# Optimization experiments

Measured on AMD Instinct MI355X. Metric: run time of the kernel, lower is better.

The kernel has to match this reference:

```python
import jax, jax.numpy as jnp
import numpy as np

D_MODEL = 1024
N_BLOCK = 20
EPS = 1e-8


def setup_inputs() -> dict:
    key = jax.random.key(0)
    k = jax.random.split(key, 7)
    B, S, D, NB = 8, 2048, D_MODEL, N_BLOCK
    e = jax.random.normal(k[0], (B, S, D), dtype=jnp.float32)
    m = jax.random.normal(k[1], (B, S, D), dtype=jnp.float32)
    state = jax.random.normal(k[2], (1, NB * D), dtype=jnp.float32)
    # learned params of the EntNet-style RNN_cell
    U = jax.random.normal(k[3], (D, D), dtype=jnp.float32) * 0.02
    V = jax.random.normal(k[4], (D, D), dtype=jnp.float32) * 0.02
    W = jax.random.normal(k[5], (D, D), dtype=jnp.float32) * 0.02
    keys = jax.random.normal(k[6], (NB, D), dtype=jnp.float32) * 0.02
    return {"e": e, "m": m, "state": state, "U": U, "V": V, "W": W, "keys": keys}


def reference(e, m, state, U, V, W, keys):
    B, S, D = e.shape
    NB = keys.shape[0]
    h0 = state.reshape(NB, D)  # shared initial memory state across batch
    x = e + m  # combined per-timestep input, (B, S, D)

    def step(h, xt):  # h: (NB, D), xt: (D,)
        # per-slot gate: content similarity + key similarity
        g = jax.nn.sigmoid(h @ xt + keys @ xt)  # (NB,)
        # candidate memory
        cand = jnp.tanh(h @ U.T + keys @ V.T + (W @ xt)[None, :])  # (NB, D)
        h = h + g[:, None] * cand
        # per-slot L2 normalization
        h = h / (jnp.linalg.norm(h, axis=1, keepdims=True) + EPS)
        return h, None

    def run(xseq):  # xseq: (S, D) -> final state (NB, D)
        hT, _ = jax.lax.scan(step, h0, xseq)
        return hT

    out = jax.vmap(run)(x)  # (B, NB, D)
    return out
```

## Files before the change

kernel.cpp:

```cpp
#include <hip/hip_runtime.h>
#include <cstdint>
#include <cstddef>

namespace {

constexpr int D   = 1024;
constexpr int NB  = 20;
constexpr int B   = 8;
constexpr int S   = 2048;
constexpr int NWG = 32;
constexpr float EPS = 1e-8f;

typedef __attribute__((ext_vector_type(4))) float f4_t;
typedef __attribute__((ext_vector_type(8))) short s8_t;
typedef unsigned long long u64_t;

__device__ __forceinline__ unsigned short f2bf(float f) {
  unsigned u = __float_as_uint(f);
  u += 0x7fffu + ((u >> 16) & 1u);
  return (unsigned short)(u >> 16);
}
__device__ __forceinline__ float bf2f(unsigned short h) {
  return __uint_as_float(((unsigned)h) << 16);
}
__device__ __forceinline__ float u64lo(u64_t x) { return __uint_as_float((unsigned)x); }
__device__ __forceinline__ float u64hi(u64_t x) { return __uint_as_float((unsigned)(x >> 32)); }
__device__ __forceinline__ float rcp_f(float x) { return __builtin_amdgcn_rcpf(x); }
__device__ __forceinline__ float sigm_fast(float x) { return rcp_f(1.0f + __expf(-x)); }
__device__ __forceinline__ float tanh_fast(float x) {
  const float e = __expf(2.0f * x);
  return 1.0f - 2.0f * rcp_f(e + 1.0f);
}

#define MFMA(a, b, c) __builtin_amdgcn_mfma_f32_16x16x32_bf16((a), (b), (c), 0, 0, 0)
#define ALOAD64(p) __hip_atomic_load((p), __ATOMIC_RELAXED, __HIP_MEMORY_SCOPE_AGENT)
#define ASTORE64(p, v) __hip_atomic_store((p), (v), __ATOMIC_RELAXED, __HIP_MEMORY_SCOPE_AGENT)
#define ALOAD32(p) __hip_atomic_load((p), __ATOMIC_RELAXED, __HIP_MEMORY_SCOPE_AGENT)
#define ASTORE32(p, v) __hip_atomic_store((p), (v), __ATOMIC_RELAXED, __HIP_MEMORY_SCOPE_AGENT)

constexpr size_t OFF_HBUF = 0;
constexpr size_t OFF_NORM = OFF_HBUF + 2ull * B * NB * 512 * 4;
constexpr size_t OFF_CTR  = OFF_NORM + 2ull * B * NB * NWG * 4;
constexpr size_t OFF_KV   = OFF_CTR + (size_t)B * 32 * 4;
constexpr size_t OFF_KX   = OFF_KV + (size_t)NB * D * 4;
constexpr size_t OFF_UHI  = OFF_KX + (size_t)B * S * NB * 4;
constexpr size_t OFF_ULO  = OFF_UHI + (size_t)D * D * 2;
constexpr size_t OFF_WHI  = OFF_ULO + (size_t)D * D * 2;
constexpr size_t OFF_WLO  = OFF_WHI + (size_t)D * D * 2;


__global__ void k_convert(const float* __restrict__ U, const float* __restrict__ W,
                          unsigned short* __restrict__ Uhi, unsigned short* __restrict__ Ulo,
                          unsigned short* __restrict__ Whi, unsigned short* __restrict__ Wlo) {
  const int n = D * D;
  for (int i = blockIdx.x * blockDim.x + threadIdx.x; i < n; i += gridDim.x * blockDim.x) {
    float u = U[i];
    unsigned short h = f2bf(u);
    Uhi[i] = h;
    Ulo[i] = f2bf(u - bf2f(h));
    float w = W[i];
    h = f2bf(w);
    Whi[i] = h;
    Wlo[i] = f2bf(w - bf2f(h));
  }
}

__global__ void k_kv(const float* __restrict__ keys, const float* __restrict__ V,
                     float* __restrict__ KV) {
  const int tid = threadIdx.x;
  const int j = blockIdx.x * 64 + (tid >> 2);
  const int kq = tid & 3;
  const f4_t* v4 = (const f4_t*)(V + (size_t)j * D + kq * 256);
  const f4_t* k4base = (const f4_t*)keys;
  float acc[NB];
#pragma unroll
  for (int i = 0; i < NB; ++i) acc[i] = 0.f;
  for (int q = 0; q < 64; ++q) {
    const f4_t v = v4[q];
#pragma unroll
    for (int i = 0; i < NB; ++i) {
      const f4_t kk = k4base[i * 256 + kq * 64 + q];
      acc[i] += kk[0] * v[0] + kk[1] * v[1] + kk[2] * v[2] + kk[3] * v[3];
    }
  }
#pragma unroll
  for (int i = 0; i < NB; ++i) {
    float s = acc[i];
    s += __shfl_xor(s, 1);
    s += __shfl_xor(s, 2);
    if (kq == 0) KV[(size_t)i * D + j] = s;
  }
}

__global__ void k_kx(const float* __restrict__ e, const float* __restrict__ m,
                     const float* __restrict__ keys, float* __restrict__ KX) {
  __shared__ f4_t xs[256];
  __shared__ float part[NB][8];
  const int bt = blockIdx.x, tid = threadIdx.x;
  xs[tid] = ((const f4_t*)e)[(size_t)bt * 256 + tid] + ((const f4_t*)m)[(size_t)bt * 256 + tid];
  __syncthreads();
  if (tid < 160) {
    const int i = tid >> 3, s8 = tid & 7;
    float acc = 0.f;
    const f4_t* k4 = (const f4_t*)keys + i * 256 + s8 * 32;
    for (int q = 0; q < 32; ++q) {
      const f4_t kk = k4[q];
      const f4_t xx = xs[s8 * 32 + q];
      acc += kk[0] * xx[0] + kk[1] * xx[1] + kk[2] * xx[2] + kk[3] * xx[3];
    }
    part[i][s8] = acc;
  }
  __syncthreads();
  if (tid < NB) {
    float s = 0.f;
#pragma unroll
    for (int q = 0; q < 8; ++q) s += part[tid][q];
    KX[(size_t)bt * NB + tid] = s;
  }
}

__global__ void k_state(const float* __restrict__ state, unsigned* __restrict__ Hbuf,
                        float* __restrict__ NormP, int* __restrict__ ctr) {
  const int idx = blockIdx.x * 256 + threadIdx.x;
  if (idx < B * NB * 512) {
    const int r = idx % (NB * 512);
    const int i = r >> 9, d2 = (r & 511) << 1;
    const unsigned short a = f2bf(state[i * D + d2]);
    const unsigned short c = f2bf(state[i * D + d2 + 1]);
    Hbuf[idx] = (unsigned)a | ((unsigned)c << 16);
  }
  const int j = idx - B * NB * 512;
  if (j >= 0 && j < B * NB * NWG) NormP[j] = 1.0f / 32.0f;
  const int q = idx - B * NB * 512 - B * NB * NWG;
  if (q >= 0 && q < B * 32) ctr[q] = 0;
}


struct __align__(16) LdsT {
  unsigned short hnA[NB * 1024];
  unsigned short xtA[2][1024];
  float credU[4][2][2][16][20];
  float wxAcc[4][2][16];
  float gAcc[4][2][16];
  float KVs[NB][32];
  float ownH[NB][32];
  float pad_force_1_block_per_cu[3072];
};

__device__ __forceinline__ void build_xt(unsigned short* xt , int tid, f4_t x) {
  const unsigned short h0 = f2bf(x[0]), h1 = f2bf(x[1]), h2 = f2bf(x[2]), h3 = f2bf(x[3]);
  const unsigned short u0 = f2bf(x[0] - bf2f(h0)), u1 = f2bf(x[1] - bf2f(h1));
  const unsigned short u2 = f2bf(x[2] - bf2f(h2)), u3 = f2bf(x[3] - bf2f(h3));
  const int kp = tid << 2;
  *(unsigned*)&xt[kp] = (unsigned)h0 | ((unsigned)h1 << 16);
  *(unsigned*)&xt[kp + 2] = (unsigned)h2 | ((unsigned)h3 << 16);
  *(unsigned*)&xt[1024 + kp] = (unsigned)u0 | ((unsigned)u1 << 16);
  *(unsigned*)&xt[1024 + kp + 2] = (unsigned)u2 | ((unsigned)u3 << 16);
}

__device__ __forceinline__ void stage_h(unsigned short* hn, int tid, const u64_t* hv) {
  const int blkk = tid >> 1;
  const int half = (tid & 1) << 2;
#pragma unroll
  for (int j = 0; j < 20; ++j)
    *(u64_t*)&hn[(j << 10) + ((blkk ^ (j & 15)) << 3) + half] = hv[j];
}

__device__ __forceinline__ void bar_lds() {
  asm volatile("s_waitcnt lgkmcnt(0)\n\ts_barrier" ::: "memory");
}
__device__ __forceinline__ void bar_full() {
  asm volatile("s_waitcnt vmcnt(0) lgkmcnt(0)\n\ts_barrier" ::: "memory");
}

__device__ __forceinline__ void poll8(const unsigned* fb, int wv, int ln, int wg,
                                      unsigned tgt) {
  const int src = (wv << 3) + (ln & 7);
  for (;;) {
    const unsigned v = (src == wg) ? tgt : ALOAD32(fb + src);
    if (__ballot(v >= tgt) == ~0ull) return;
    __builtin_amdgcn_s_sleep(1);
  }
}

__device__ __forceinline__ void poll32(const unsigned* fb, int ln31, int wg,
                                       unsigned tgt, unsigned pv) {
  if (__ballot(pv >= tgt) == ~0ull) return;
  for (;;) {
    const unsigned v = (ln31 == wg) ? tgt : ALOAD32(fb + ln31);
    if (__ballot(v >= tgt) == ~0ull) return;
    __builtin_amdgcn_s_sleep(1);
  }
}

__launch_bounds__(256, 1)
__global__ void k_rnn(const float* __restrict__ e, const float* __restrict__ m,
                      const float* __restrict__ state,
                      const float* __restrict__ KX, const float* __restrict__ KV,
                      const unsigned short* __restrict__ Uhi, const unsigned short* __restrict__ Ulo,
                      const unsigned short* __restrict__ Whi, const unsigned short* __restrict__ Wlo,
                      unsigned* __restrict__ Hbuf, float* __restrict__ NormP,
                      int* __restrict__ ctr, float* __restrict__ out) {
  __shared__ LdsT L;
  const int tid = threadIdx.x;
  const int b = blockIdx.x >> 5;
  const int wg = blockIdx.x & 31;
  const int wv = tid >> 6;
  const int ln = tid & 63;
  const int l15 = ln & 15;
  const int lo4 = ln >> 4;
  const int ln31 = tid & 31;
  const int r1 = 16 + (l15 < 4 ? l15 : 3);
  unsigned* ctrp = (unsigned*)ctr + b * 32;

  const bool uact = (ln < 40);
  const int ui = wv * 5 + (ln >> 3);
  const int uc4 = (ln & 7) << 2;

  s8_t BUh[2][8], BUl[2][8], BWh[2][8], BWl[2][8];
  {
    const int rowb = (wg << 5) + l15;
#pragma unroll
    for (int nt = 0; nt < 2; ++nt)
#pragma unroll
      for (int kf = 0; kf < 8; ++kf) {
        const size_t off = (size_t)(rowb + nt * 16) * D + (wv << 8) + (kf << 5) + (lo4 << 3);
        BUh[nt][kf] = *(const s8_t*)(Uhi + off);
        BUl[nt][kf] = *(const s8_t*)(Ulo + off);
        BWh[nt][kf] = *(const s8_t*)(Whi + off);
        BWl[nt][kf] = *(const s8_t*)(Wlo + off);
      }
  }
  if (tid < 160) {
    const int i = tid >> 3, c4 = (tid & 7) << 2;
    *(f4_t*)&L.ownH[i][c4] = *(const f4_t*)(state + (size_t)i * D + (wg << 5) + c4);
    *(f4_t*)&L.KVs[i][c4] = *(const f4_t*)(KV + (size_t)i * D + (wg << 5) + c4);
  }

  f4_t evv, mvv;
  float sreg = 1.f;
  float kxreg = 0.f;

  s8_t AX[8], A0r[8], A1r[8];
  f4_t cWa0 = {0, 0, 0, 0}, cWa1 = {0, 0, 0, 0};
  f4_t cGa0 = {0, 0, 0, 0}, cGa1 = {0, 0, 0, 0};

  {
    u64_t hv[20];
    const u64_t* hb8 = (const u64_t*)Hbuf + (size_t)(0 * B + b) * (NB * 256);
#pragma unroll
    for (int j = 0; j < 20; ++j) hv[j] = ALOAD64(hb8 + j * 256 + tid);
    const f4_t x0 = ((const f4_t*)e)[(size_t)(b * S) * 256 + tid] +
                    ((const f4_t*)m)[(size_t)(b * S) * 256 + tid];
    build_xt(&L.xtA[0][0], tid, x0);
    stage_h(L.hnA, tid, hv);
    if (uact) kxreg = KX[(size_t)(b * S) * NB + ui];
    evv = ((const f4_t*)e)[(size_t)(b * S + 1) * 256 + tid];
    mvv = ((const f4_t*)m)[(size_t)(b * S + 1) * 256 + tid];
    asm volatile("s_waitcnt lgkmcnt(0)" ::: "memory");
    const unsigned short* xb = &L.xtA[0][0];
    const unsigned short* hb = L.hnA;
#pragma unroll
    for (int kf = 0; kf < 8; ++kf) {
      const int blk = (wv << 5) + (kf << 2) + lo4;
      AX[kf] = *(const s8_t*)&xb[(l15 & 1) * 1024 + (blk << 3)];
      A0r[kf] = *(const s8_t*)&hb[(l15 << 10) + ((blk ^ l15) << 3)];
      A1r[kf] = *(const s8_t*)&hb[(r1 << 10) + ((blk ^ (r1 & 15)) << 3)];
    }
#pragma unroll
    for (int kf = 0; kf < 8; ++kf) {
      cWa0 = MFMA(AX[kf], BWh[0][kf], cWa0);
      cWa0 = MFMA(AX[kf], BWl[0][kf], cWa0);
      cWa1 = MFMA(AX[kf], BWh[1][kf], cWa1);
      cWa1 = MFMA(AX[kf], BWl[1][kf], cWa1);
      cGa0 = MFMA(AX[kf], A0r[kf], cGa0);
      cGa1 = MFMA(AX[kf], A1r[kf], cGa1);
    }
  }
  __syncthreads();

  for (int t = 0; t < S; ++t) {
    const int nxt2 = (t + 1) & 1;

    f4_t cU00 = {0, 0, 0, 0}, cU01 = {0, 0, 0, 0}, cU10 = {0, 0, 0, 0}, cU11 = {0, 0, 0, 0};
#pragma unroll
    for (int kf = 0; kf < 8; ++kf) {
      cU00 = MFMA(A0r[kf], BUh[0][kf], cU00);
      cU00 = MFMA(A0r[kf], BUl[0][kf], cU00);
      cU01 = MFMA(A0r[kf], BUh[1][kf], cU01);
      cU01 = MFMA(A0r[kf], BUl[1][kf], cU01);
      cU10 = MFMA(A1r[kf], BUh[0][kf], cU10);
      cU10 = MFMA(A1r[kf], BUl[0][kf], cU10);
      cU11 = MFMA(A1r[kf], BUh[1][kf], cU11);
      cU11 = MFMA(A1r[kf], BUl[1][kf], cU11);
    }
#pragma unroll
    for (int q = 0; q < 4; ++q) {
      const int r = (lo4 << 2) + q;
      L.credU[wv][0][0][r][l15] = cU00[q];
      L.credU[wv][0][1][r][l15] = cU01[q];
      L.credU[wv][1][0][r][l15] = cU10[q];
      L.credU[wv][1][1][r][l15] = cU11[q];
    }
    if (lo4 == 0) {
      L.wxAcc[wv][0][l15] = cWa0[0] + cWa0[1];
      L.wxAcc[wv][1][l15] = cWa1[0] + cWa1[1];
      L.gAcc[wv][0][l15] = cGa0[0] + cGa0[1];
      L.gAcc[wv][1][l15] = cGa1[0] + cGa1[1];
    }
    bar_lds();

    unsigned pv = 0;
    if (t + 1 < S) pv = (ln31 == wg) ? (unsigned)(t + 1) : ALOAD32(ctrp + ln31);

    if (uact) {
      const int i = ui, c4 = uc4;
      const int mt = i >> 4, r = i & 15, nt = c4 >> 4, ccc = c4 & 15;
      const f4_t sU = *(const f4_t*)&L.credU[0][mt][nt][r][ccc] +
                      *(const f4_t*)&L.credU[1][mt][nt][r][ccc] +
                      *(const f4_t*)&L.credU[2][mt][nt][r][ccc] +
                      *(const f4_t*)&L.credU[3][mt][nt][r][ccc];
      const f4_t wx = *(const f4_t*)&L.wxAcc[0][nt][ccc] +
                      *(const f4_t*)&L.wxAcc[1][nt][ccc] +
                      *(const f4_t*)&L.wxAcc[2][nt][ccc] +
                      *(const f4_t*)&L.wxAcc[3][nt][ccc];
      const f4_t kv = *(const f4_t*)&L.KVs[i][c4];
      const f4_t oh = *(const f4_t*)&L.ownH[i][c4];
      const float s = sreg;
      const float gpre = s * (L.gAcc[0][mt][r] + L.gAcc[1][mt][r] +
                              L.gAcc[2][mt][r] + L.gAcc[3][mt][r]) + kxreg;
      const float g = sigm_fast(gpre);
      f4_t hn;
      float sq = 0.f;
#pragma unroll
      for (int u = 0; u < 4; ++u) {
        const float cand = tanh_fast(s * sU[u] + kv[u] + wx[u]);
        const float hx = s * oh[u] + g * cand;
        hn[u] = hx;
        sq += hx * hx;
      }
      *(f4_t*)&L.ownH[i][c4] = hn;
      const unsigned d0 = (unsigned)f2bf(hn[0]) | ((unsigned)f2bf(hn[1]) << 16);
      const unsigned d1 = (unsigned)f2bf(hn[2]) | ((unsigned)f2bf(hn[3]) << 16);
      u64_t* hb8 = (u64_t*)Hbuf + (size_t)(nxt2 * B + b) * (NB * 256) +
                   (i << 8) + (wg << 3) + (c4 >> 2);
      ASTORE64(hb8, (u64_t)d0 | ((u64_t)d1 << 32));
      sq += __shfl_xor(sq, 1);
      sq += __shfl_xor(sq, 2);
      sq += __shfl_xor(sq, 4);
      if ((ln & 7) == 0) {
        unsigned* np = (unsigned*)NormP + ((size_t)(nxt2 * B + b) * NB + i) * NWG + wg;
        ASTORE32(np, __float_as_uint(sq));
      }
    }
    bar_full();

    if (tid == 0) ASTORE32(ctrp + wg, (unsigned)(t + 1));

    if (t + 1 < S) {
      poll8(ctrp, wv, ln, wg, (unsigned)(t + 1));
      u64_t hv[20];
      const u64_t* g0 = (const u64_t*)Hbuf + (size_t)(nxt2 * B + b) * (NB * 256);
#pragma unroll
      for (int j = 0; j < 20; ++j) hv[j] = ALOAD64(g0 + j * 256 + tid);
      build_xt(&L.xtA[0][0], tid, evv + mvv);
      asm volatile("s_waitcnt lgkmcnt(0)" ::: "memory");
      {
        const unsigned short* xb = &L.xtA[0][0];
#pragma unroll
        for (int kf = 0; kf < 8; ++kf) {
          const int blk = (wv << 5) + (kf << 2) + lo4;
          AX[kf] = *(const s8_t*)&xb[(l15 & 1) * 1024 + (blk << 3)];
        }
        cWa0 = (f4_t){0, 0, 0, 0};
        cWa1 = (f4_t){0, 0, 0, 0};
#pragma unroll
        for (int kf = 0; kf < 8; ++kf) {
          cWa0 = MFMA(AX[kf], BWh[0][kf], cWa0);
          cWa0 = MFMA(AX[kf], BWl[0][kf], cWa0);
          cWa1 = MFMA(AX[kf], BWh[1][kf], cWa1);
          cWa1 = MFMA(AX[kf], BWl[1][kf], cWa1);
        }
      }
      poll32(ctrp, ln31, wg, (unsigned)(t + 1), pv);
      float np0 = 0.f;
      if (uact) {
        const u64_t* n0 = (const u64_t*)NormP + ((size_t)(nxt2 * B + b) * NB + ui) * 16 + ((ln & 7) << 1);
        const u64_t a0 = ALOAD64(n0);
        const u64_t a1 = ALOAD64(n0 + 1);
        np0 = u64lo(a0) + u64hi(a0) + u64lo(a1) + u64hi(a1);
        kxreg = KX[((size_t)b * S + t + 1) * NB + ui];
      }
      stage_h(L.hnA, tid, hv);
      if (t + 2 < S) {
        evv = ((const f4_t*)e)[(size_t)(b * S + t + 2) * 256 + tid];
        mvv = ((const f4_t*)m)[(size_t)(b * S + t + 2) * 256 + tid];
      }
      asm volatile("s_waitcnt lgkmcnt(0)" ::: "memory");
      {
        const unsigned short* hb = L.hnA;
#pragma unroll
        for (int kf = 0; kf < 8; ++kf) {
          const int blk = (wv << 5) + (kf << 2) + lo4;
          A0r[kf] = *(const s8_t*)&hb[(l15 << 10) + ((blk ^ l15) << 3)];
          A1r[kf] = *(const s8_t*)&hb[(r1 << 10) + ((blk ^ (r1 & 15)) << 3)];
        }
        cGa0 = (f4_t){0, 0, 0, 0};
        cGa1 = (f4_t){0, 0, 0, 0};
#pragma unroll
        for (int kf = 0; kf < 8; ++kf) {
          cGa0 = MFMA(AX[kf], A0r[kf], cGa0);
          cGa1 = MFMA(AX[kf], A1r[kf], cGa1);
        }
      }
      if (uact) {
        float s0 = np0;
        s0 += __shfl_xor(s0, 1);
        s0 += __shfl_xor(s0, 2);
        s0 += __shfl_xor(s0, 4);
        sreg = rcp_f(sqrtf(s0) + EPS);
      }
    }
  }

  poll32(ctrp, ln31, wg, (unsigned)S, 0u);
  if (uact) {
    const int i = ui, c4 = uc4;
    const u64_t* np8 = (const u64_t*)NormP + ((size_t)(0 * B + b) * NB + i) * 16 + ((ln & 7) << 1);
    const u64_t x0 = ALOAD64(np8);
    const u64_t x1 = ALOAD64(np8 + 1);
    float sq = u64lo(x0) + u64hi(x0) + u64lo(x1) + u64hi(x1);
    sq += __shfl_xor(sq, 1);
    sq += __shfl_xor(sq, 2);
    sq += __shfl_xor(sq, 4);
    const float sc = rcp_f(sqrtf(sq) + EPS);
    const f4_t oh = *(const f4_t*)&L.ownH[i][c4];
    f4_t ov;
#pragma unroll
    for (int u = 0; u < 4; ++u) ov[u] = sc * oh[u];
    *(f4_t*)(out + (size_t)b * NB * D + (size_t)i * D + (wg << 5) + c4) = ov;
  }
}

}

extern "C" void kernel_launch(void* const* d_in, const int* in_sizes, int n_in,
                              void* d_out, int out_size, void* d_ws, size_t ws_size,
                              hipStream_t stream) {
  const float* e = (const float*)d_in[0];
  const float* m = (const float*)d_in[1];
  const float* state = (const float*)d_in[2];
  const float* U = (const float*)d_in[3];
  const float* V = (const float*)d_in[4];
  const float* W = (const float*)d_in[5];
  const float* keys = (const float*)d_in[6];
  float* out = (float*)d_out;
  char* ws = (char*)d_ws;

  unsigned* Hbuf = (unsigned*)(ws + OFF_HBUF);
  float* NormP = (float*)(ws + OFF_NORM);
  int* ctr = (int*)(ws + OFF_CTR);
  float* KV = (float*)(ws + OFF_KV);
  float* KX = (float*)(ws + OFF_KX);
  unsigned short* Uhi = (unsigned short*)(ws + OFF_UHI);
  unsigned short* Ulo = (unsigned short*)(ws + OFF_ULO);
  unsigned short* Whi = (unsigned short*)(ws + OFF_WHI);
  unsigned short* Wlo = (unsigned short*)(ws + OFF_WLO);

  k_convert<<<512, 256, 0, stream>>>(U, W, Uhi, Ulo, Whi, Wlo);
  k_kv<<<16, 256, 0, stream>>>(keys, V, KV);
  k_kx<<<B * S, 256, 0, stream>>>(e, m, keys, KX);
  k_state<<<342, 256, 0, stream>>>(state, Hbuf, NormP, ctr);
  k_rnn<<<B * NWG, 256, 0, stream>>>(e, m, state, KX, KV, Uhi, Ulo, Whi, Wlo,
                                     Hbuf, NormP, ctr, out);
}
```

Baseline: 11.50 ms.

## Replace post-update barrier with LDS atomic counter and double-buffer reduction scratch

Removes the full workgroup barrier after the per-step state update. Instead, each wave drains its global stores and increments an LDS counter, and the last of the four waves publishes the cross-workgroup progress flag. The LDS reduction buffers (credU, wxAcc, gAcc) become double-buffered by step parity so the next step's writes cannot clobber data still being read. The LDS padding that forced one block per CU is also dropped. The ordering of the counter reset and the flag store depends on relaxed atomics, which risks subtle races.

```diff
diff --git a/kernel.cpp b/kernel.cpp
--- a/kernel.cpp
+++ b/kernel.cpp
@@ -139,12 +139,12 @@
 struct __align__(16) LdsT {
   unsigned short hnA[NB * 1024];
   unsigned short xtA[2][1024];
-  float credU[4][2][2][16][20];
-  float wxAcc[4][2][16];
-  float gAcc[4][2][16];
+  float credU[2][4][2][2][16][20];
+  float wxAcc[2][4][2][16];
+  float gAcc[2][4][2][16];
   float KVs[NB][32];
   float ownH[NB][32];
-  float pad_force_1_block_per_cu[3072];
+  unsigned cnt;
 };
 
 __device__ __forceinline__ void build_xt(unsigned short* xt , int tid, f4_t x) {
@@ -168,9 +168,6 @@
 
 __device__ __forceinline__ void bar_lds() {
   asm volatile("s_waitcnt lgkmcnt(0)\n\ts_barrier" ::: "memory");
-}
-__device__ __forceinline__ void bar_full() {
-  asm volatile("s_waitcnt vmcnt(0) lgkmcnt(0)\n\ts_barrier" ::: "memory");
 }
 
 __device__ __forceinline__ void poll8(const unsigned* fb, int wv, int ln, int wg,
@@ -236,6 +233,7 @@
     *(f4_t*)&L.ownH[i][c4] = *(const f4_t*)(state + (size_t)i * D + (wg << 5) + c4);
     *(f4_t*)&L.KVs[i][c4] = *(const f4_t*)(KV + (size_t)i * D + (wg << 5) + c4);
   }
+  if (tid == 0) L.cnt = 0u;
 
   f4_t evv, mvv;
   float sreg = 1.f;
@@ -281,6 +279,7 @@
 
   for (int t = 0; t < S; ++t) {
     const int nxt2 = (t + 1) & 1;
+    const int p = t & 1;
 
     f4_t cU00 = {0, 0, 0, 0}, cU01 = {0, 0, 0, 0}, cU10 = {0, 0, 0, 0}, cU11 = {0, 0, 0, 0};
 #pragma unroll
@@ -297,16 +296,16 @@
 #pragma unroll
     for (int q = 0; q < 4; ++q) {
       const int r = (lo4 << 2) + q;
-      L.credU[wv][0][0][r][l15] = cU00[q];
-      L.credU[wv][0][1][r][l15] = cU01[q];
-      L.credU[wv][1][0][r][l15] = cU10[q];
-      L.credU[wv][1][1][r][l15] = cU11[q];
+      L.credU[p][wv][0][0][r][l15] = cU00[q];
+      L.credU[p][wv][0][1][r][l15] = cU01[q];
+      L.credU[p][wv][1][0][r][l15] = cU10[q];
+      L.credU[p][wv][1][1][r][l15] = cU11[q];
     }
     if (lo4 == 0) {
-      L.wxAcc[wv][0][l15] = cWa0[0] + cWa0[1];
-      L.wxAcc[wv][1][l15] = cWa1[0] + cWa1[1];
-      L.gAcc[wv][0][l15] = cGa0[0] + cGa0[1];
-      L.gAcc[wv][1][l15] = cGa1[0] + cGa1[1];
+      L.wxAcc[p][wv][0][l15] = cWa0[0] + cWa0[1];
+      L.wxAcc[p][wv][1][l15] = cWa1[0] + cWa1[1];
+      L.gAcc[p][wv][0][l15] = cGa0[0] + cGa0[1];
+      L.gAcc[p][wv][1][l15] = cGa1[0] + cGa1[1];
     }
     bar_lds();
 
@@ -316,19 +315,19 @@
     if (uact) {
       const int i = ui, c4 = uc4;
       const int mt = i >> 4, r = i & 15, nt = c4 >> 4, ccc = c4 & 15;
-      const f4_t sU = *(const f4_t*)&L.credU[0][mt][nt][r][ccc] +
-                      *(const f4_t*)&L.credU[1][mt][nt][r][ccc] +
-                      *(const f4_t*)&L.credU[2][mt][nt][r][ccc] +
-                      *(const f4_t*)&L.credU[3][mt][nt][r][ccc];
-      const f4_t wx = *(const f4_t*)&L.wxAcc[0][nt][ccc] +
-                      *(const f4_t*)&L.wxAcc[1][nt][ccc] +
-                      *(const f4_t*)&L.wxAcc[2][nt][ccc] +
-                      *(const f4_t*)&L.wxAcc[3][nt][ccc];
+      const f4_t sU = *(const f4_t*)&L.credU[p][0][mt][nt][r][ccc] +
+                      *(const f4_t*)&L.credU[p][1][mt][nt][r][ccc] +
+                      *(const f4_t*)&L.credU[p][2][mt][nt][r][ccc] +
+                      *(const f4_t*)&L.credU[p][3][mt][nt][r][ccc];
+      const f4_t wx = *(const f4_t*)&L.wxAcc[p][0][nt][ccc] +
+                      *(const f4_t*)&L.wxAcc[p][1][nt][ccc] +
+                      *(const f4_t*)&L.wxAcc[p][2][nt][ccc] +
+                      *(const f4_t*)&L.wxAcc[p][3][nt][ccc];
       const f4_t kv = *(const f4_t*)&L.KVs[i][c4];
       const f4_t oh = *(const f4_t*)&L.ownH[i][c4];
       const float s = sreg;
-      const float gpre = s * (L.gAcc[0][mt][r] + L.gAcc[1][mt][r] +
-                              L.gAcc[2][mt][r] + L.gAcc[3][mt][r]) + kxreg;
+      const float gpre = s * (L.gAcc[p][0][mt][r] + L.gAcc[p][1][mt][r] +
+                              L.gAcc[p][2][mt][r] + L.gAcc[p][3][mt][r]) + kxreg;
       const float g = sigm_fast(gpre);
       f4_t hn;
       float sq = 0.f;
@@ -353,9 +352,16 @@
         ASTORE32(np, __float_as_uint(sq));
       }
     }
-    bar_full();
-
-    if (tid == 0) ASTORE32(ctrp + wg, (unsigned)(t + 1));
+
+    asm volatile("s_waitcnt vmcnt(0)" ::: "memory");
+    if (ln == 0) {
+      const unsigned old = __hip_atomic_fetch_add(&L.cnt, 1u, __ATOMIC_RELAXED,
+                                                  __HIP_MEMORY_SCOPE_WORKGROUP);
+      if (old == 3u) {
+        L.cnt = 0u;
+        ASTORE32(ctrp + wg, (unsigned)(t + 1));
+      }
+    }
 
     if (t + 1 < S) {
       poll8(ctrp, wv, ln, wg, (unsigned)(t + 1));
```

After: 14.18 ms. 1.23x slower.
